# Kernel optimization log

Measured on AMD Instinct MI355X. Metric: run time of the kernel, lower is better.

Reference implementation:

```python
import jax, jax.numpy as jnp
import numpy as np

B, L, IDIM = 2, 4096, 2048
N_HEADS, N_GROUPS, HEAD_DIM = 16, 4, 128
GROUP_SIZE = N_HEADS // N_GROUPS
WINDOW = 1024
SCALE = 256.0 ** -0.5  # query_pre_attn_scalar = 256
EPS = 1e-6


def setup_inputs() -> dict:
    key = jax.random.key(0)
    ks = jax.random.split(key, 8)
    x = jax.random.normal(ks[0], (B, L, IDIM), dtype=jnp.float32)
    # realistic RoPE tables
    inv_freq = 1.0 / (10000.0 ** (np.arange(0, HEAD_DIM, 2, dtype=np.float32) / HEAD_DIM))
    t = np.arange(L, dtype=np.float32)
    freqs = np.outer(t, inv_freq)                      # [L, HEAD_DIM//2]
    emb = np.concatenate([freqs, freqs], axis=-1)      # [L, HEAD_DIM]
    cos = jnp.asarray(np.cos(emb), dtype=jnp.float32)
    sin = jnp.asarray(np.sin(emb), dtype=jnp.float32)
    s = 0.02
    Wq = jax.random.normal(ks[1], (IDIM, N_HEADS * HEAD_DIM), dtype=jnp.float32) * s
    Wk = jax.random.normal(ks[2], (IDIM, N_GROUPS * HEAD_DIM), dtype=jnp.float32) * s
    Wv = jax.random.normal(ks[3], (IDIM, N_GROUPS * HEAD_DIM), dtype=jnp.float32) * s
    Wo = jax.random.normal(ks[4], (N_HEADS * HEAD_DIM, IDIM), dtype=jnp.float32) * s
    qn_w = jnp.ones((HEAD_DIM,), dtype=jnp.float32)
    kn_w = jnp.ones((HEAD_DIM,), dtype=jnp.float32)
    return {"x": x, "cos": cos, "sin": sin, "Wq": Wq, "Wk": Wk, "Wv": Wv, "Wo": Wo, "qn_w": qn_w, "kn_w": kn_w}


def _rmsnorm(x, w):
    var = jnp.mean(jnp.square(x), axis=-1, keepdims=True)
    return x * jax.lax.rsqrt(var + EPS) * w


def _rope(x, cos, sin):
    # x: [b, h, l, d]; cos/sin: [l, d]
    d2 = x.shape[-1] // 2
    x1, x2 = x[..., :d2], x[..., d2:]
    rot = jnp.concatenate([-x2, x1], axis=-1)
    return x * cos[None, None] + rot * sin[None, None]


def reference(x, cos, sin, Wq, Wk, Wv, Wo, qn_w, kn_w):
    b, l, _ = x.shape
    q = (x @ Wq).reshape(b, l, N_HEADS, HEAD_DIM).transpose(0, 2, 1, 3)   # b h l d
    k = (x @ Wk).reshape(b, l, N_GROUPS, HEAD_DIM).transpose(0, 2, 1, 3)  # b g l d
    v = (x @ Wv).reshape(b, l, N_GROUPS, HEAD_DIM).transpose(0, 2, 1, 3)  # b g l d
    q = _rmsnorm(q, qn_w)
    k = _rmsnorm(k, kn_w)
    q = _rope(q, cos, sin)
    k = _rope(k, cos, sin)
    k = jnp.repeat(k, GROUP_SIZE, axis=1)  # b h l d
    v = jnp.repeat(v, GROUP_SIZE, axis=1)
    dots = jnp.einsum('bhid,bhjd->bhij', q, k) * SCALE
    i = jnp.arange(l)[:, None]
    j = jnp.arange(l)[None, :]
    allowed = (j <= i) & (j > i - WINDOW)  # causal sliding window
    dots = jnp.where(allowed[None, None], dots, -jnp.inf)
    attn = jax.nn.softmax(dots, axis=-1)
    out = jnp.einsum('bhij,bhjd->bhid', attn, v)
    out = out.transpose(0, 2, 1, 3).reshape(b, l, N_HEADS * HEAD_DIM)
    return out @ Wo
```

## Files before the change

### kernel.cpp

```cpp
#include <hip/hip_runtime.h>
#include <hip/hip_bf16.h>

typedef __hip_bfloat16 bf16;
typedef __attribute__((ext_vector_type(8))) __bf16 bf16x8;
typedef __attribute__((ext_vector_type(4))) float f32x4;

#define MFMA16(a, b, c) __builtin_amdgcn_mfma_f32_16x16x32_bf16((a), (b), (c), 0, 0, 0)

static __device__ __forceinline__ void gload_lds16(const void* g, void* l) {
    typedef const __attribute__((address_space(1))) unsigned gq_t;
    typedef __attribute__((address_space(3))) unsigned ls_t;
    __builtin_amdgcn_global_load_lds((gq_t*)g, (ls_t*)l, 16, 0, 0);
}

static __device__ __forceinline__ unsigned short f2bfbits(float f) {
    bf16 h = __float2bfloat16(f);
    return *reinterpret_cast<unsigned short*>(&h);
}

__global__ __launch_bounds__(256) void prep_kernel(const float* __restrict__ x,
                                                   const float* __restrict__ Wq,
                                                   const float* __restrict__ Wk,
                                                   const float* __restrict__ Wv,
                                                   const float* __restrict__ Wo,
                                                   bf16* __restrict__ xb,
                                                   bf16* __restrict__ wqkvT,
                                                   bf16* __restrict__ woT) {
    __shared__ float tile[32][33];
    int t = threadIdx.x;
    int blk = blockIdx.x;
    if (blk < 8192) {
        int i = (blk * 256 + t) * 8;
        float4 a = *reinterpret_cast<const float4*>(x + i);
        float4 b = *reinterpret_cast<const float4*>(x + i + 4);
        bf16 tmp[8];
        tmp[0] = __float2bfloat16(a.x); tmp[1] = __float2bfloat16(a.y);
        tmp[2] = __float2bfloat16(a.z); tmp[3] = __float2bfloat16(a.w);
        tmp[4] = __float2bfloat16(b.x); tmp[5] = __float2bfloat16(b.y);
        tmp[6] = __float2bfloat16(b.z); tmp[7] = __float2bfloat16(b.w);
        *reinterpret_cast<uint4*>(xb + i) = *reinterpret_cast<const uint4*>(tmp);
    } else if (blk < 14336) {
        int bid = blk - 8192;
        int k0 = (bid & 63) * 32;
        int n0 = (bid >> 6) * 32;
        int tx = t & 31, ty = t >> 5;
#pragma unroll
        for (int i = 0; i < 4; ++i) {
            int k = k0 + ty + i * 8, n = n0 + tx;
            float v;
            if (n < 2048)      v = Wq[(size_t)k * 2048 + n];
            else if (n < 2560) v = Wk[(size_t)k * 512 + (n - 2048)];
            else               v = Wv[(size_t)k * 512 + (n - 2560)];
            tile[ty + i * 8][tx] = v;
        }
        __syncthreads();
#pragma unroll
        for (int i = 0; i < 4; ++i)
            wqkvT[(size_t)(n0 + ty + i * 8) * 2048 + k0 + tx] = __float2bfloat16(tile[tx][ty + i * 8]);
    } else {
        int bid = blk - 14336;
        int k0 = (bid & 63) * 32, n0 = (bid >> 6) * 32;
        int tx = t & 31, ty = t >> 5;
#pragma unroll
        for (int i = 0; i < 4; ++i)
            tile[ty + i * 8][tx] = Wo[(size_t)(k0 + ty + i * 8) * 2048 + n0 + tx];
        __syncthreads();
#pragma unroll
        for (int i = 0; i < 4; ++i)
            woT[(size_t)(n0 + ty + i * 8) * 2048 + k0 + tx] = __float2bfloat16(tile[tx][ty + i * 8]);
    }
}

template <int NFRAG, bool OUT_F32>
__global__ __launch_bounds__(512, 4) void gemmocc_kernel(const bf16* __restrict__ A,
                                                         const bf16* __restrict__ BT,
                                                         void* __restrict__ Cv,
                                                         int M, int N, int K, int nbn) {
    constexpr int BN = NFRAG * 64;
    constexpr int PB = NFRAG;
    __shared__ bf16 As[2][128 * 64];
    __shared__ bf16 Bs[2][BN * 64];
    int t = threadIdx.x;
    int lane = t & 63, w = t >> 6;
    int wm = w >> 2, wn = w & 3;
    int lr = lane & 15, lq = lane >> 4;
    int lin = blockIdx.x;
    int xcd = lin & 7;
    int local = lin >> 3;
    int grp = local >> 3;
    int wit = local & 7;
    int g_bm = (grp / (nbn >> 2)) << 1;
    int g_bn = (grp % (nbn >> 2)) << 2;
    int bm = xcd * 8 + g_bm + (wit >> 2);
    int bn = g_bn + (wit & 3);
    const bf16* Ab = A + (size_t)bm * 128 * K;
    const bf16* Bb = BT + (size_t)bn * BN * K;

    auto stA = [&](int slot, int kt, int piece) {
        int idx = piece * 512 + t;
        int r = idx >> 3, c8 = idx & 7;
        gload_lds16(Ab + (size_t)r * K + kt * 64 + ((c8 ^ (r & 7)) * 8), &As[slot][idx * 8]);
    };
    auto stB = [&](int slot, int kt, int piece) {
        int idx = piece * 512 + t;
        int r = idx >> 3, c8 = idx & 7;
        gload_lds16(Bb + (size_t)r * K + kt * 64 + ((c8 ^ (r & 7)) * 8), &Bs[slot][idx * 8]);
    };

    f32x4 acc[4][NFRAG] = {};
    bf16x8 bq[NFRAG][2], af[2][2];

    auto readB = [&](int slot) {
#pragma unroll
        for (int n = 0; n < NFRAG; ++n)
#pragma unroll
            for (int ks = 0; ks < 2; ++ks) {
                int ro = wn * (NFRAG * 16) + n * 16 + lr;
                int ch = (ks * 4 + lq) ^ (ro & 7);
                bq[n][ks] = *reinterpret_cast<const bf16x8*>(&Bs[slot][ro * 64 + ch * 8]);
            }
    };
    auto readA = [&](int mbase, int slot) {
#pragma unroll
        for (int mi = 0; mi < 2; ++mi)
#pragma unroll
            for (int ks = 0; ks < 2; ++ks) {
                int ro = wm * 64 + (mbase + mi) * 16 + lr;
                int ch = (ks * 4 + lq) ^ (ro & 7);
                af[mi][ks] = *reinterpret_cast<const bf16x8*>(&As[slot][ro * 64 + ch * 8]);
            }
    };
    auto mf = [&](int mbase) {
#pragma unroll
        for (int mi = 0; mi < 2; ++mi)
#pragma unroll
            for (int n = 0; n < NFRAG; ++n)
#pragma unroll
                for (int ks = 0; ks < 2; ++ks)
                    acc[mbase + mi][n] = MFMA16(af[mi][ks], bq[n][ks], acc[mbase + mi][n]);
    };

#define GATE_PB() asm volatile("s_waitcnt vmcnt(%0)" :: "i"(PB) : "memory")
#define PHASE_TAIL()                                                       \
    do {                                                                   \
        __builtin_amdgcn_s_barrier();                                      \
        asm volatile("s_waitcnt lgkmcnt(0)" ::: "memory");                 \
    } while (0)
#define MFMA_CLUSTER(mb)                                                   \
    do {                                                                   \
        __builtin_amdgcn_s_setprio(1);                                     \
        mf(mb);                                                            \
        __builtin_amdgcn_s_setprio(0);                                     \
        __builtin_amdgcn_s_barrier();                                      \
    } while (0)

    int nkt = K >> 6;
    stA(0, 0, 0); stA(0, 0, 1);
#pragma unroll
    for (int p = 0; p < PB; ++p) stB(0, 0, p);
#pragma unroll
    for (int p = 0; p < PB; ++p) stB(1, 1, p);
    GATE_PB();
    __builtin_amdgcn_s_barrier();

    int nI = nkt >> 1;
    for (int I = 0; I < nI; ++I) {
        int T = I << 1;
        bool s2 = (T + 2) < nkt;
        readB(0); readA(0, 0);
        stA(1, T + 1, 0); stA(1, T + 1, 1);
        PHASE_TAIL();
        MFMA_CLUSTER(0);
        readA(2, 0);
        if (s2) {
#pragma unroll
            for (int p = 0; p < PB; ++p) stB(0, T + 2, p);
            GATE_PB();
        } else {
            asm volatile("s_waitcnt vmcnt(0)" ::: "memory");
        }
        PHASE_TAIL();
        MFMA_CLUSTER(2);
        readB(1); readA(0, 1);
        if (s2) { stA(0, T + 2, 0); stA(0, T + 2, 1); }
        PHASE_TAIL();
        MFMA_CLUSTER(0);
        readA(2, 1);
        if (s2) {
#pragma unroll
            for (int p = 0; p < PB; ++p) stB(1, T + 3, p);
            GATE_PB();
        } else {
            asm volatile("s_waitcnt vmcnt(0)" ::: "memory");
        }
        PHASE_TAIL();
        MFMA_CLUSTER(2);
    }
#undef GATE_PB
#undef PHASE_TAIL
#undef MFMA_CLUSTER

#pragma unroll
    for (int m = 0; m < 4; ++m)
#pragma unroll
        for (int n = 0; n < NFRAG; ++n) {
            int row = bm * 128 + wm * 64 + m * 16 + lq * 4;
            int col = bn * BN + wn * (NFRAG * 16) + n * 16 + lr;
#pragma unroll
            for (int j = 0; j < 4; ++j) {
                if (OUT_F32)
                    ((float*)Cv)[(size_t)(row + j) * N + col] = acc[m][n][j];
                else
                    ((bf16*)Cv)[(size_t)(row + j) * N + col] = __float2bfloat16(acc[m][n][j]);
            }
        }
}

__global__ __launch_bounds__(256) void normrope_vtrans_kernel(const bf16* __restrict__ qkv,
                                                              const float* __restrict__ cosT,
                                                              const float* __restrict__ sinT,
                                                              const float* __restrict__ qnw,
                                                              const float* __restrict__ knw,
                                                              bf16* __restrict__ qh,
                                                              bf16* __restrict__ kh,
                                                              bf16* __restrict__ vt) {
    __shared__ bf16 tile[64][132];
    int t = threadIdx.x;
    int blk = blockIdx.x;
    if (blk < 40960) {
        int lane = t & 63, wv = t >> 6;
        int r = blk / 5;
        int s = (blk % 5) * 4 + wv;
        int b = r >> 12, l = r & 4095;
        int e0 = lane * 2;
        const bf16* src = qkv + (size_t)r * 3072 + s * 128;
        ushort2 xu = *reinterpret_cast<const ushort2*>(src + e0);
        float v0 = __uint_as_float((unsigned)xu.x << 16);
        float v1 = __uint_as_float((unsigned)xu.y << 16);
        float ss = v0 * v0 + v1 * v1;
#pragma unroll
        for (int d = 1; d < 64; d <<= 1) ss += __shfl_xor(ss, d, 64);
        float rn = rsqrtf(ss * (1.0f / 128.0f) + 1e-6f);
        const float* wn = (s < 16) ? qnw : knw;
        float2 wv2 = *reinterpret_cast<const float2*>(wn + e0);
        float xn0 = v0 * rn * wv2.x;
        float xn1 = v1 * rn * wv2.y;
        float xp0 = __shfl_xor(xn0, 32, 64);
        float xp1 = __shfl_xor(xn1, 32, 64);
        float r0 = (lane < 32) ? -xp0 : xp0;
        float r1 = (lane < 32) ? -xp1 : xp1;
        float2 c2 = *reinterpret_cast<const float2*>(cosT + (size_t)l * 128 + e0);
        float2 s2 = *reinterpret_cast<const float2*>(sinT + (size_t)l * 128 + e0);
        float o0 = xn0 * c2.x + r0 * s2.x;
        float o1 = xn1 * c2.y + r1 * s2.y;
        ushort2 ou;
        if (s < 16) {
            const float scl = 0.0625f * 1.44269504088896f;
            ou.x = f2bfbits(o0 * scl);
            ou.y = f2bfbits(o1 * scl);
            bf16* dst = qh + ((size_t)(b * 16 + s) * 4096 + l) * 128;
            *reinterpret_cast<ushort2*>(dst + e0) = ou;
        } else {
            int g = s - 16;
            ou.x = f2bfbits(o0);
            ou.y = f2bfbits(o1);
            int sw = (l & 7) << 3;
            bf16* dst = kh + ((size_t)(b * 4 + g) * 4096 + l) * 128;
            *reinterpret_cast<ushort2*>(dst + (e0 ^ sw)) = ou;
        }
    } else {
        int bid2 = blk - 40960;
        int l0 = (bid2 & 63) * 64;
        int bg = bid2 >> 6;
        int b = bg >> 2, g = bg & 3;
        const bf16* src = qkv + ((size_t)(b * 4096 + l0)) * 3072 + 2560 + g * 128;
#pragma unroll
        for (int i = 0; i < 4; ++i) {
            int c = i * 256 + t;
            int r = c >> 4, c16 = c & 15;
            uint4 v = *reinterpret_cast<const uint4*>(src + (size_t)r * 3072 + c16 * 8);
            *reinterpret_cast<uint2*>(&tile[r][c16 * 8]) = make_uint2(v.x, v.y);
            *reinterpret_cast<uint2*>(&tile[r][c16 * 8 + 4]) = make_uint2(v.z, v.w);
        }
        __syncthreads();
        bf16* dst = vt + (size_t)bg * 128 * 4096 + l0;
        int cj = t & 63;
        int pos = (cj & 0x23) | ((cj & 16) >> 2) | ((cj & 12) << 1);
#pragma unroll
        for (int dd = 0; dd < 32; ++dd) {
            int d = (t >> 6) * 32 + dd;
            dst[(size_t)d * 4096 + (pos ^ ((d & 7) << 3))] = tile[cj][d];
        }
    }
}

__global__ __launch_bounds__(256, 2) void attn_kernel(const bf16* __restrict__ qh,
                                                      const bf16* __restrict__ kh,
                                                      const bf16* __restrict__ vt,
                                                      bf16* __restrict__ ao) {
    __shared__ bf16 Ks[2][64 * 128];
    __shared__ bf16 Vs[2][128 * 64];
    int t = threadIdx.x;
    int lane = t & 63, w = t >> 6;
    int lr = lane & 15, lq = lane >> 4;
    int bid = blockIdx.x;
    int bh = (bid & 7) * 4 + (bid >> 8);
    int qi_chunk = 31 - ((bid >> 3) & 31);
    int qs = qi_chunk * 128;
    int b = bh >> 4, h = bh & 15, g = (h >> 2) & 3;
    int row0 = qs + w * 32;
    const bf16* qp = qh + ((size_t)(b * 16 + h) * 4096 + row0) * 128;
    const bf16* kp = kh + (size_t)(b * 4 + g) * 4096 * 128;
    const bf16* vp = vt + (size_t)(b * 4 + g) * 128 * 4096;

    bf16x8 aq[2][4];
#pragma unroll
    for (int g2 = 0; g2 < 2; ++g2)
#pragma unroll
        for (int kk = 0; kk < 4; ++kk)
            aq[g2][kk] = *reinterpret_cast<const bf16x8*>(qp + (size_t)(g2 * 16 + lr) * 128 + kk * 32 + lq * 8);

    union { unsigned short u[8]; bf16x8 v; } onesu;
#pragma unroll
    for (int k = 0; k < 8; ++k) onesu.u[k] = 0x3F80;
    bf16x8 ones = onesu.v;

    const float SH = 11.5415603f;
    f32x4 o0[8] = {}, o1[8] = {};
    f32x4 osum0 = {}, osum1 = {};
    int qi0 = row0 + lr, qi1 = row0 + 16 + lr;
    int sA = max(0, row0 - 1023) >> 6;
    int sB = max(0, row0 + 16 - 1023) >> 6;
    int t1w = row0 >> 6;
    int t0w = sA;
    int t0 = max(0, qs - 1023) >> 6;
    int t1 = (qs + 127) >> 6;

    auto stage = [&](int buf, int kt) {
        int j0 = kt * 64;
        const bf16* kg = kp + (size_t)j0 * 128;
#pragma unroll
        for (int i = 0; i < 4; ++i) {
            int c = i * 256 + t;
            gload_lds16(kg + c * 8, &Ks[buf][c * 8]);
        }
#pragma unroll
        for (int i = 0; i < 4; ++i) {
            int c = i * 256 + t;
            int d = c >> 3, co = (c & 7) * 8;
            gload_lds16(vp + (size_t)d * 4096 + j0 + co, &Vs[buf][c * 8]);
        }
    };

    stage(0, t0);
    int cur = 0;

    for (int kt = t0; kt <= t1; ++kt) {
        asm volatile("s_waitcnt vmcnt(0)" ::: "memory");
        __builtin_amdgcn_s_barrier();
        if (kt < t1) stage(cur ^ 1, kt + 1);
        if (kt >= t0w && kt <= t1w) {
            int j0 = kt * 64;
            f32x4 s0[4], s1[4];
#pragma unroll
            for (int jt = 0; jt < 4; ++jt) {
                s0[jt][0] = -SH; s0[jt][1] = -SH; s0[jt][2] = -SH; s0[jt][3] = -SH;
                s1[jt][0] = -SH; s1[jt][1] = -SH; s1[jt][2] = -SH; s1[jt][3] = -SH;
            }
            __builtin_amdgcn_s_setprio(1);
#pragma unroll
            for (int jt = 0; jt < 4; ++jt) {
                int r = jt * 16 + lr;
                int rs = (r & 7) << 3;
#pragma unroll
                for (int kk = 0; kk < 4; ++kk) {
                    int c = kk * 32 + lq * 8;
                    bf16x8 bk = *reinterpret_cast<const bf16x8*>(&Ks[cur][r * 128 + (c ^ rs)]);
                    s0[jt] = MFMA16(bk, aq[0][kk], s0[jt]);
                    s1[jt] = MFMA16(bk, aq[1][kk], s1[jt]);
                }
            }
            __builtin_amdgcn_s_setprio(0);
            if (kt <= sA + 1 || kt == t1w) {
#pragma unroll
                for (int jt = 0; jt < 4; ++jt)
#pragma unroll
                    for (int j = 0; j < 4; ++j) {
                        int kj = j0 + jt * 16 + lq * 4 + j;
                        if (!(kj <= qi0 && kj > qi0 - 1024)) s0[jt][j] = -1e30f;
                    }
            }
            if (kt <= sB + 1 || kt == t1w) {
#pragma unroll
                for (int jt = 0; jt < 4; ++jt)
#pragma unroll
                    for (int j = 0; j < 4; ++j) {
                        int kj = j0 + jt * 16 + lq * 4 + j;
                        if (!(kj <= qi1 && kj > qi1 - 1024)) s1[jt][j] = -1e30f;
                    }
            }
            unsigned pk0[4][2], pk1[4][2];
#pragma unroll
            for (int jt = 0; jt < 4; ++jt)
#pragma unroll
                for (int hh = 0; hh < 2; ++hh) {
                    float p0 = __builtin_amdgcn_exp2f(s0[jt][2 * hh]);
                    float p1 = __builtin_amdgcn_exp2f(s0[jt][2 * hh + 1]);
                    asm("v_cvt_pk_bf16_f32 %0, %1, %2" : "=v"(pk0[jt][hh]) : "v"(p0), "v"(p1));
                }
#pragma unroll
            for (int jt = 0; jt < 4; ++jt)
#pragma unroll
                for (int hh = 0; hh < 2; ++hh) {
                    float p0 = __builtin_amdgcn_exp2f(s1[jt][2 * hh]);
                    float p1 = __builtin_amdgcn_exp2f(s1[jt][2 * hh + 1]);
                    asm("v_cvt_pk_bf16_f32 %0, %1, %2" : "=v"(pk1[jt][hh]) : "v"(p0), "v"(p1));
                }
            __builtin_amdgcn_s_setprio(1);
#pragma unroll
            for (int kk2 = 0; kk2 < 2; ++kk2) {
                union { unsigned u[4]; bf16x8 v; } pu0, pu1;
                pu0.u[0] = pk0[2 * kk2][0]; pu0.u[1] = pk0[2 * kk2][1];
                pu0.u[2] = pk0[2 * kk2 + 1][0]; pu0.u[3] = pk0[2 * kk2 + 1][1];
                pu1.u[0] = pk1[2 * kk2][0]; pu1.u[1] = pk1[2 * kk2][1];
                pu1.u[2] = pk1[2 * kk2 + 1][0]; pu1.u[3] = pk1[2 * kk2 + 1][1];
                osum0 = MFMA16(pu0.v, ones, osum0);
                osum1 = MFMA16(pu1.v, ones, osum1);
#pragma unroll
                for (int dt = 0; dt < 8; ++dt) {
                    int r = dt * 16 + lr;
                    int c = kk2 * 32 + lq * 8;
                    bf16x8 bv = *reinterpret_cast<const bf16x8*>(&Vs[cur][r * 64 + (c ^ ((r & 7) << 3))]);
                    o0[dt] = MFMA16(pu0.v, bv, o0[dt]);
                    o1[dt] = MFMA16(pu1.v, bv, o1[dt]);
                }
            }
            __builtin_amdgcn_s_setprio(0);
        }
        cur ^= 1;
    }
    float lv0[4], lv1[4];
#pragma unroll
    for (int j = 0; j < 4; ++j) {
        lv0[j] = 1.0f / osum0[j];
        lv1[j] = 1.0f / osum1[j];
    }
#pragma unroll
    for (int dt = 0; dt < 8; ++dt)
#pragma unroll
        for (int j = 0; j < 4; ++j) {
            size_t base = (size_t)(b * 4096 + row0 + lq * 4 + j) * 2048 + h * 128 + dt * 16 + lr;
            ao[base] = __float2bfloat16(o0[dt][j] * lv0[j]);
            ao[base + (size_t)16 * 2048] = __float2bfloat16(o1[dt][j] * lv1[j]);
        }
}

extern "C" void kernel_launch(void* const* d_in, const int* in_sizes, int n_in,
                              void* d_out, int out_size, void* d_ws, size_t ws_size,
                              hipStream_t stream) {
    const float* x    = (const float*)d_in[0];
    const float* cosT = (const float*)d_in[1];
    const float* sinT = (const float*)d_in[2];
    const float* Wq   = (const float*)d_in[3];
    const float* Wk   = (const float*)d_in[4];
    const float* Wv   = (const float*)d_in[5];
    const float* Wo   = (const float*)d_in[6];
    const float* qnw  = (const float*)d_in[7];
    const float* knw  = (const float*)d_in[8];

    char* ws = (char*)d_ws;
    bf16* xb    = (bf16*)(ws);
    bf16* wqkvT = (bf16*)(ws + 33554432);
    bf16* woT   = (bf16*)(ws + 46137344);
    bf16* qh    = (bf16*)(ws + 54525952);
    bf16* kh    = (bf16*)(ws + 88080384);
    bf16* vt    = (bf16*)(ws + 96468992);
    bf16* ao    = xb;
    bf16* qkv   = (bf16*)d_out;

    prep_kernel<<<18432, 256, 0, stream>>>(x, Wq, Wk, Wv, Wo, xb, wqkvT, woT);
    gemmocc_kernel<3, false><<<1024, 512, 0, stream>>>(xb, wqkvT, (void*)qkv, 8192, 3072, 2048, 16);
    normrope_vtrans_kernel<<<41472, 256, 0, stream>>>(qkv, cosT, sinT, qnw, knw, qh, kh, vt);
    attn_kernel<<<1024, 256, 0, stream>>>(qh, kh, vt, ao);
    gemmocc_kernel<2, true><<<1024, 512, 0, stream>>>(ao, woT, d_out, 8192, 2048, 2048, 16);
}
```

Measured before the change: 301.1 us.

## Use 4-wave GEMM blocks with each wave covering all 128 rows

The GEMM kernel now runs with 256 threads (4 waves) instead of 512. Each wave owns a full 128-row by NFRAG*16-column strip, so it holds 8xNFRAG accumulators and reuses each loaded B fragment across twice as many MFMAs. The k-step pipeline is stretched to four MFMA clusters per slot, and the B-tile loads are split across two phases. This cuts LDS fragment reads per MFMA and the number of waves per block, at the cost of more registers per wave and lower occupancy (launch bounds change to 256,2).

```diff
diff --git a/kernel.cpp b/kernel.cpp
--- a/kernel.cpp
+++ b/kernel.cpp
@@ -72,17 +72,17 @@
 }
 
 template <int NFRAG, bool OUT_F32>
-__global__ __launch_bounds__(512, 4) void gemmocc_kernel(const bf16* __restrict__ A,
-                                                         const bf16* __restrict__ BT,
-                                                         void* __restrict__ Cv,
-                                                         int M, int N, int K, int nbn) {
+__global__ __launch_bounds__(256, 2) void gemmwide_kernel(const bf16* __restrict__ A,
+                                                          const bf16* __restrict__ BT,
+                                                          void* __restrict__ Cv,
+                                                          int M, int N, int K, int nbn) {
     constexpr int BN = NFRAG * 64;
     constexpr int PB = NFRAG;
+    constexpr int PB2 = 2 * NFRAG;
     __shared__ bf16 As[2][128 * 64];
     __shared__ bf16 Bs[2][BN * 64];
     int t = threadIdx.x;
     int lane = t & 63, w = t >> 6;
-    int wm = w >> 2, wn = w & 3;
     int lr = lane & 15, lq = lane >> 4;
     int lin = blockIdx.x;
     int xcd = lin & 7;
@@ -97,17 +97,17 @@
     const bf16* Bb = BT + (size_t)bn * BN * K;
 
     auto stA = [&](int slot, int kt, int piece) {
-        int idx = piece * 512 + t;
+        int idx = piece * 256 + t;
         int r = idx >> 3, c8 = idx & 7;
         gload_lds16(Ab + (size_t)r * K + kt * 64 + ((c8 ^ (r & 7)) * 8), &As[slot][idx * 8]);
     };
     auto stB = [&](int slot, int kt, int piece) {
-        int idx = piece * 512 + t;
+        int idx = piece * 256 + t;
         int r = idx >> 3, c8 = idx & 7;
         gload_lds16(Bb + (size_t)r * K + kt * 64 + ((c8 ^ (r & 7)) * 8), &Bs[slot][idx * 8]);
     };
 
-    f32x4 acc[4][NFRAG] = {};
+    f32x4 acc[8][NFRAG] = {};
     bf16x8 bq[NFRAG][2], af[2][2];
 
     auto readB = [&](int slot) {
@@ -115,7 +115,7 @@
         for (int n = 0; n < NFRAG; ++n)
 #pragma unroll
             for (int ks = 0; ks < 2; ++ks) {
-                int ro = wn * (NFRAG * 16) + n * 16 + lr;
+                int ro = w * (NFRAG * 16) + n * 16 + lr;
                 int ch = (ks * 4 + lq) ^ (ro & 7);
                 bq[n][ks] = *reinterpret_cast<const bf16x8*>(&Bs[slot][ro * 64 + ch * 8]);
             }
@@ -125,7 +125,7 @@
         for (int mi = 0; mi < 2; ++mi)
 #pragma unroll
             for (int ks = 0; ks < 2; ++ks) {
-                int ro = wm * 64 + (mbase + mi) * 16 + lr;
+                int ro = (mbase + mi) * 16 + lr;
                 int ch = (ks * 4 + lq) ^ (ro & 7);
                 af[mi][ks] = *reinterpret_cast<const bf16x8*>(&As[slot][ro * 64 + ch * 8]);
             }
@@ -140,7 +140,7 @@
                     acc[mbase + mi][n] = MFMA16(af[mi][ks], bq[n][ks], acc[mbase + mi][n]);
     };
 
-#define GATE_PB() asm volatile("s_waitcnt vmcnt(%0)" :: "i"(PB) : "memory")
+#define GATE_PB2() asm volatile("s_waitcnt vmcnt(%0)" :: "i"(PB2) : "memory")
 #define PHASE_TAIL()                                                       \
     do {                                                                   \
         __builtin_amdgcn_s_barrier();                                      \
@@ -155,12 +155,13 @@
     } while (0)
 
     int nkt = K >> 6;
-    stA(0, 0, 0); stA(0, 0, 1);
-#pragma unroll
-    for (int p = 0; p < PB; ++p) stB(0, 0, p);
-#pragma unroll
-    for (int p = 0; p < PB; ++p) stB(1, 1, p);
-    GATE_PB();
+#pragma unroll
+    for (int p = 0; p < 4; ++p) stA(0, 0, p);
+#pragma unroll
+    for (int p = 0; p < PB2; ++p) stB(0, 0, p);
+#pragma unroll
+    for (int p = 0; p < PB2; ++p) stB(1, 1, p);
+    GATE_PB2();
     __builtin_amdgcn_s_barrier();
 
     int nI = nkt >> 1;
@@ -168,44 +169,66 @@
         int T = I << 1;
         bool s2 = (T + 2) < nkt;
         readB(0); readA(0, 0);
-        stA(1, T + 1, 0); stA(1, T + 1, 1);
+#pragma unroll
+        for (int p = 0; p < 4; ++p) stA(1, T + 1, p);
         PHASE_TAIL();
         MFMA_CLUSTER(0);
         readA(2, 0);
         if (s2) {
 #pragma unroll
             for (int p = 0; p < PB; ++p) stB(0, T + 2, p);
-            GATE_PB();
-        } else {
-            asm volatile("s_waitcnt vmcnt(0)" ::: "memory");
         }
         PHASE_TAIL();
         MFMA_CLUSTER(2);
+        readA(4, 0);
+        if (s2) {
+#pragma unroll
+            for (int p = PB; p < PB2; ++p) stB(0, T + 2, p);
+        }
+        PHASE_TAIL();
+        MFMA_CLUSTER(4);
+        readA(6, 0);
+        if (s2) GATE_PB2();
+        else    asm volatile("s_waitcnt vmcnt(0)" ::: "memory");
+        PHASE_TAIL();
+        MFMA_CLUSTER(6);
         readB(1); readA(0, 1);
-        if (s2) { stA(0, T + 2, 0); stA(0, T + 2, 1); }
+        if (s2) {
+#pragma unroll
+            for (int p = 0; p < 4; ++p) stA(0, T + 2, p);
+        }
         PHASE_TAIL();
         MFMA_CLUSTER(0);
         readA(2, 1);
         if (s2) {
 #pragma unroll
             for (int p = 0; p < PB; ++p) stB(1, T + 3, p);
-            GATE_PB();
-        } else {
-            asm volatile("s_waitcnt vmcnt(0)" ::: "memory");
         }
         PHASE_TAIL();
         MFMA_CLUSTER(2);
+        readA(4, 1);
+        if (s2) {
+#pragma unroll
+            for (int p = PB; p < PB2; ++p) stB(1, T + 3, p);
+        }
+        PHASE_TAIL();
+        MFMA_CLUSTER(4);
+        readA(6, 1);
+        if (s2) GATE_PB2();
+        else    asm volatile("s_waitcnt vmcnt(0)" ::: "memory");
+        PHASE_TAIL();
+        MFMA_CLUSTER(6);
     }
-#undef GATE_PB
+#undef GATE_PB2
 #undef PHASE_TAIL
 #undef MFMA_CLUSTER
 
 #pragma unroll
-    for (int m = 0; m < 4; ++m)
+    for (int m = 0; m < 8; ++m)
 #pragma unroll
         for (int n = 0; n < NFRAG; ++n) {
-            int row = bm * 128 + wm * 64 + m * 16 + lq * 4;
-            int col = bn * BN + wn * (NFRAG * 16) + n * 16 + lr;
+            int row = bm * 128 + m * 16 + lq * 4;
+            int col = bn * BN + w * (NFRAG * 16) + n * 16 + lr;
 #pragma unroll
             for (int j = 0; j < 4; ++j) {
                 if (OUT_F32)
@@ -479,8 +502,8 @@
     bf16* qkv   = (bf16*)d_out;
 
     prep_kernel<<<18432, 256, 0, stream>>>(x, Wq, Wk, Wv, Wo, xb, wqkvT, woT);
-    gemmocc_kernel<3, false><<<1024, 512, 0, stream>>>(xb, wqkvT, (void*)qkv, 8192, 3072, 2048, 16);
+    gemmwide_kernel<3, false><<<1024, 256, 0, stream>>>(xb, wqkvT, (void*)qkv, 8192, 3072, 2048, 16);
     normrope_vtrans_kernel<<<41472, 256, 0, stream>>>(qkv, cosT, sinT, qnw, knw, qh, kh, vt);
     attn_kernel<<<1024, 256, 0, stream>>>(qh, kh, vt, ao);
-    gemmocc_kernel<2, true><<<1024, 512, 0, stream>>>(ao, woT, d_out, 8192, 2048, 2048, 16);
-}
+    gemmwide_kernel<2, true><<<1024, 256, 0, stream>>>(ao, woT, d_out, 8192, 2048, 2048, 16);
+}
```

After: 312.1 us. +3.6%, slower.
